# Optimization experiments

Measured on AMD Instinct MI355X. Metric: run time of the kernel, lower is better.

The kernel has to match this reference:

```python
import jax, jax.numpy as jnp
import numpy as np

D_MODEL = 768
N_HEADS = 12
D_K = D_MODEL // N_HEADS
B, S = 2, 2048
EPS = 1e-5  # torch LayerNorm default


def setup_inputs() -> dict:
    key = jax.random.key(0)
    ks = jax.random.split(key, 12)
    sc = 1.0 / np.sqrt(D_MODEL)
    inp = {
        "q": jax.random.normal(ks[0], (B, S, D_MODEL), jnp.float32),
        "k": jax.random.normal(ks[1], (B, S, D_MODEL), jnp.float32),
        "v": jax.random.normal(ks[2], (B, S, D_MODEL), jnp.float32),
        # causal mask: 1 = keep, 0 = masked
        "mask": jnp.tril(jnp.ones((S, S), jnp.int32))[None, None, :, :],
        "Wq": jax.random.normal(ks[3], (D_MODEL, D_MODEL), jnp.float32) * sc,
        "bq": jnp.zeros((D_MODEL,), jnp.float32),
        "Wk": jax.random.normal(ks[4], (D_MODEL, D_MODEL), jnp.float32) * sc,
        "bk": jnp.zeros((D_MODEL,), jnp.float32),
        "Wv": jax.random.normal(ks[5], (D_MODEL, D_MODEL), jnp.float32) * sc,
        "bv": jnp.zeros((D_MODEL,), jnp.float32),
        "Wo": jax.random.normal(ks[6], (D_MODEL, D_MODEL), jnp.float32) * sc,
        "bo": jnp.zeros((D_MODEL,), jnp.float32),
        "gamma": jnp.ones((D_MODEL,), jnp.float32),
        "beta": jnp.zeros((D_MODEL,), jnp.float32),
    }
    return inp


def _layernorm(x, gamma, beta):
    mu = jnp.mean(x, axis=-1, keepdims=True)
    var = jnp.mean(jnp.square(x - mu), axis=-1, keepdims=True)
    return (x - mu) * jax.lax.rsqrt(var + EPS) * gamma + beta


def reference(q, k, v, mask, Wq, bq, Wk, bk, Wv, bv, Wo, bo, gamma, beta):
    residual = q
    # projections + split heads: [B,S,D] -> [B,H,S,Dk]
    def split_heads(x):
        return x.reshape(B, S, N_HEADS, D_K).transpose(0, 2, 1, 3)
    Q = split_heads(q @ Wq.T + bq)
    K = split_heads(k @ Wk.T + bk)
    V = split_heads(v @ Wv.T + bv)
    scores = jnp.einsum("bhqd,bhkd->bhqk", Q, K) / jnp.sqrt(jnp.float32(D_K))
    scores = jnp.where(mask == 0, -jnp.inf, scores)
    attn = jax.nn.softmax(scores, axis=-1)
    # dropout is identity in eval mode
    out = jnp.einsum("bhqk,bhkd->bhqd", attn, V)
    out = out.transpose(0, 2, 1, 3).reshape(B, S, D_MODEL)
    out = out @ Wo.T + bo
    out = _layernorm(residual + out, gamma, beta)
    return (out, attn)
```

## Files before the change

### kernel.cpp

```cpp
#include <hip/hip_runtime.h>
#include <math.h>

typedef __attribute__((ext_vector_type(8))) short bf8_t;
typedef __attribute__((ext_vector_type(4))) float f4_t;

#define MFMA(a,b,c) __builtin_amdgcn_mfma_f32_16x16x32_bf16(a,b,c,0,0,0)

static constexpr int S_ = 2048;
static constexpr size_t QKV_ELEMS = 3145728;
static constexpr size_t W_ELEMS   = 589824;
static constexpr size_t OUT0_ELEMS = 3145728;

__device__ __forceinline__ unsigned short f2bf(float f) {
    union { float f; unsigned u; } v; v.f = f;
    unsigned u = v.u;
    u += 0x7fffu + ((u >> 16) & 1u);
    return (unsigned short)(u >> 16);
}

struct CvtP { const float* s[7]; unsigned short* d[7]; int n[7]; };

__global__ __launch_bounds__(256)
void cvt_all(CvtP p)
{
    const int z = blockIdx.z;
    const int i = (blockIdx.x * 256 + threadIdx.x) * 8;
    if (i >= p.n[z]) return;
    const float* s = p.s[z] + i;
    float4 a = *(const float4*)s, b = *(const float4*)(s + 4);
    uint4 u;
    u.x = (unsigned)f2bf(a.x) | ((unsigned)f2bf(a.y) << 16);
    u.y = (unsigned)f2bf(a.z) | ((unsigned)f2bf(a.w) << 16);
    u.z = (unsigned)f2bf(b.x) | ((unsigned)f2bf(b.y) << 16);
    u.w = (unsigned)f2bf(b.z) | ((unsigned)f2bf(b.w) << 16);
    *(uint4*)(p.d[z] + i) = u;
}

struct GemmP {
    const short* A[3]; const short* W[3]; const float* bias[3];
    void* C[3]; float scale[3]; int mode[3];
};

__global__ __launch_bounds__(256)
void gemm_bf16(GemmP p)
{
    const int z = blockIdx.z;
    const short* __restrict__ A = p.A[z];
    const short* __restrict__ W = p.W[z];
    const float* __restrict__ bias = p.bias[z];
    const float scale = p.scale[z];
    const int mode = p.mode[z];

    __shared__ short As[128 * 40];
    __shared__ short Bs[128 * 40];

    const int t = threadIdx.x;
    const int m0 = blockIdx.y * 128, n0 = blockIdx.x * 128;
    const int w = t >> 6, lane = t & 63, li = lane & 15, qd = lane >> 4;
    const int wm = (w & 1) * 64, wn = (w >> 1) * 64;

    f4_t acc[4][4];
    #pragma unroll
    for (int i = 0; i < 4; ++i)
        #pragma unroll
        for (int j = 0; j < 4; ++j)
            #pragma unroll
            for (int r = 0; r < 4; ++r) acc[i][j][r] = 0.f;

    for (int k0 = 0; k0 < 768; k0 += 32) {
        #pragma unroll
        for (int e = 0; e < 2; ++e) {
            int v = t + e * 256;
            int r = v >> 2, c = (v & 3) * 8;
            *(float4*)&As[r * 40 + c] = *(const float4*)&A[(size_t)(m0 + r) * 768 + k0 + c];
            *(float4*)&Bs[r * 40 + c] = *(const float4*)&W[(size_t)(n0 + r) * 768 + k0 + c];
        }
        __syncthreads();
        bf8_t af[4], bf[4];
        #pragma unroll
        for (int i = 0; i < 4; ++i) af[i] = *(const bf8_t*)&As[(wm + i * 16 + li) * 40 + qd * 8];
        #pragma unroll
        for (int j = 0; j < 4; ++j) bf[j] = *(const bf8_t*)&Bs[(wn + j * 16 + li) * 40 + qd * 8];
        #pragma unroll
        for (int i = 0; i < 4; ++i)
            #pragma unroll
            for (int j = 0; j < 4; ++j)
                acc[i][j] = MFMA(af[i], bf[j], acc[i][j]);
        __syncthreads();
    }

    #pragma unroll
    for (int i = 0; i < 4; ++i) {
        const int row = m0 + wm + i * 16 + qd * 4;
        #pragma unroll
        for (int j = 0; j < 4; ++j) {
            const int col = n0 + wn + j * 16 + li;
            const float bv = bias[col];
            float vals[4];
            #pragma unroll
            for (int r = 0; r < 4; ++r) vals[r] = (acc[i][j][r] + bv) * scale;
            if (mode == 0) {
                #pragma unroll
                for (int r = 0; r < 4; ++r) {
                    const int rr = row + r;
                    int bh = (rr >> 11) * 12 + (col >> 6);
                    ((unsigned short*)p.C[z])[((size_t)bh * 2048 + (rr & 2047)) * 64 + (col & 63)] = f2bf(vals[r]);
                }
            } else if (mode == 1) {
                int bh = (row >> 11) * 12 + (col >> 6);
                ushort4 u;
                u.x = f2bf(vals[0]); u.y = f2bf(vals[1]);
                u.z = f2bf(vals[2]); u.w = f2bf(vals[3]);
                *(ushort4*)&((unsigned short*)p.C[z])[(size_t)(bh * 64 + (col & 63)) * 2048 + (row & 2047)] = u;
            } else {
                #pragma unroll
                for (int r = 0; r < 4; ++r)
                    ((float*)p.C[z])[(size_t)(row + r) * 768 + col] = vals[r];
            }
        }
    }
}

__global__ __launch_bounds__(256)
void attn_fused(const short* __restrict__ Qb, const short* __restrict__ Kb,
                const short* __restrict__ Vt, float* __restrict__ attn,
                unsigned short* __restrict__ AO)
{
    const int qt = 31 - blockIdx.x;
    const int bh = blockIdx.y;
    const int t = threadIdx.x;
    const int ws = t >> 6;
    const int lane = t & 63;
    const int li = lane & 15, qd = lane >> 4;

    __shared__ short Ks[2][4096];
    __shared__ short Vs[2][4096];
    __shared__ short Ps[4][1024];

    const int q0 = qt * 64 + ws * 16;
    const short* Qp = Qb + ((size_t)bh * 2048 + q0 + li) * 64;
    const bf8_t qf0 = *(const bf8_t*)&Qp[qd * 8];
    const bf8_t qf1 = *(const bf8_t*)&Qp[32 + qd * 8];

    const short* Kbh = Kb + (size_t)bh * 2048 * 64;
    const short* Vbh = Vt + (size_t)bh * 64 * 2048;
    float* attnp = attn + (size_t)bh * 2048 * 2048;
    short* Psw = Ps[ws];

    const int r0 = t >> 3, c0 = t & 7;
    const int csw = ((c0 ^ (r0 & 7)) << 3);
    const int lsw = li & 7;

    const float NEG = -1e30f;
    float m_[4] = {NEG, NEG, NEG, NEG}, l_[4] = {0.f, 0.f, 0.f, 0.f};

    {
        float4 ka = *(const float4*)&Kbh[(size_t)r0 * 64 + (c0 << 3)];
        float4 kb_ = *(const float4*)&Kbh[(size_t)(r0 + 32) * 64 + (c0 << 3)];
        *(float4*)&Ks[0][r0 * 64 + csw] = ka;
        *(float4*)&Ks[0][(r0 + 32) * 64 + csw] = kb_;
        int cur = 0;
        for (int kt = 0; kt <= qt; ++kt) {
            float4 na, nb;
            if (kt < qt) {
                na = *(const float4*)&Kbh[(size_t)((kt + 1) * 64 + r0) * 64 + (c0 << 3)];
                nb = *(const float4*)&Kbh[(size_t)((kt + 1) * 64 + r0 + 32) * 64 + (c0 << 3)];
            }
            __syncthreads();
            const short* Kc = Ks[cur];
            bf8_t kf0[4], kf1[4];
            #pragma unroll
            for (int sub = 0; sub < 4; ++sub) {
                const int kr = sub * 16 + li;
                kf0[sub] = *(const bf8_t*)&Kc[kr * 64 + ((qd ^ lsw) << 3)];
                kf1[sub] = *(const bf8_t*)&Kc[kr * 64 + (((4 + qd) ^ lsw) << 3)];
            }
            f4_t c[4];
            #pragma unroll
            for (int sub = 0; sub < 4; ++sub) {
                f4_t z; z[0] = z[1] = z[2] = z[3] = 0.f;
                z = MFMA(qf0, kf0[sub], z);
                z = MFMA(qf1, kf1[sub], z);
                c[sub] = z;
            }
            if (kt == qt) {
                #pragma unroll
                for (int sub = 0; sub < 4; ++sub)
                    #pragma unroll
                    for (int r = 0; r < 4; ++r)
                        if (sub * 16 + li > ws * 16 + qd * 4 + r) c[sub][r] = NEG;
            }
            #pragma unroll
            for (int r = 0; r < 4; ++r) {
                float tm = fmaxf(fmaxf(c[0][r], c[1][r]), fmaxf(c[2][r], c[3][r]));
                float nm = fmaxf(m_[r], tm);
                float s = __expf(c[0][r] - nm) + __expf(c[1][r] - nm)
                        + __expf(c[2][r] - nm) + __expf(c[3][r] - nm);
                l_[r] = l_[r] * __expf(m_[r] - nm) + s;
                m_[r] = nm;
            }
            if (kt < qt) {
                *(float4*)&Ks[cur ^ 1][r0 * 64 + csw] = na;
                *(float4*)&Ks[cur ^ 1][(r0 + 32) * 64 + csw] = nb;
                cur ^= 1;
            }
        }
    }

    float invl[4];
    #pragma unroll
    for (int r = 0; r < 4; ++r) {
        float mg = m_[r];
        mg = fmaxf(mg, __shfl_xor(mg, 1, 64));
        mg = fmaxf(mg, __shfl_xor(mg, 2, 64));
        mg = fmaxf(mg, __shfl_xor(mg, 4, 64));
        mg = fmaxf(mg, __shfl_xor(mg, 8, 64));
        float lg = l_[r] * __expf(m_[r] - mg);
        lg += __shfl_xor(lg, 1, 64);
        lg += __shfl_xor(lg, 2, 64);
        lg += __shfl_xor(lg, 4, 64);
        lg += __shfl_xor(lg, 8, 64);
        m_[r] = mg;
        invl[r] = 1.f / lg;
    }

    f4_t o[4];
    #pragma unroll
    for (int d = 0; d < 4; ++d)
        #pragma unroll
        for (int r = 0; r < 4; ++r) o[d][r] = 0.f;

    {
        float4 ka = *(const float4*)&Kbh[(size_t)r0 * 64 + (c0 << 3)];
        float4 kb_ = *(const float4*)&Kbh[(size_t)(r0 + 32) * 64 + (c0 << 3)];
        float4 va = *(const float4*)&Vbh[(size_t)r0 * 2048 + (c0 << 3)];
        float4 vc_ = *(const float4*)&Vbh[(size_t)(r0 + 32) * 2048 + (c0 << 3)];
        __syncthreads();
        *(float4*)&Ks[0][r0 * 64 + csw] = ka;
        *(float4*)&Ks[0][(r0 + 32) * 64 + csw] = kb_;
        *(float4*)&Vs[0][r0 * 64 + csw] = va;
        *(float4*)&Vs[0][(r0 + 32) * 64 + csw] = vc_;
        int cur = 0;
        for (int kt = 0; kt <= qt; ++kt) {
            float4 nka, nkb, nva, nvb;
            if (kt < qt) {
                nka = *(const float4*)&Kbh[(size_t)((kt + 1) * 64 + r0) * 64 + (c0 << 3)];
                nkb = *(const float4*)&Kbh[(size_t)((kt + 1) * 64 + r0 + 32) * 64 + (c0 << 3)];
                nva = *(const float4*)&Vbh[(size_t)r0 * 2048 + (kt + 1) * 64 + (c0 << 3)];
                nvb = *(const float4*)&Vbh[(size_t)(r0 + 32) * 2048 + (kt + 1) * 64 + (c0 << 3)];
            }
            __syncthreads();
            const short* Kc = Ks[cur];
            const short* Vc = Vs[cur];
            bf8_t kf0[4], kf1[4];
            #pragma unroll
            for (int sub = 0; sub < 4; ++sub) {
                const int kr = sub * 16 + li;
                kf0[sub] = *(const bf8_t*)&Kc[kr * 64 + ((qd ^ lsw) << 3)];
                kf1[sub] = *(const bf8_t*)&Kc[kr * 64 + (((4 + qd) ^ lsw) << 3)];
            }
            f4_t c[4];
            #pragma unroll
            for (int sub = 0; sub < 4; ++sub) {
                f4_t z; z[0] = z[1] = z[2] = z[3] = 0.f;
                z = MFMA(qf0, kf0[sub], z);
                z = MFMA(qf1, kf1[sub], z);
                c[sub] = z;
            }
            if (kt == qt) {
                #pragma unroll
                for (int sub = 0; sub < 4; ++sub)
                    #pragma unroll
                    for (int r = 0; r < 4; ++r)
                        if (sub * 16 + li > ws * 16 + qd * 4 + r) c[sub][r] = NEG;
            }
            #pragma unroll
            for (int sub = 0; sub < 4; ++sub)
                #pragma unroll
                for (int r = 0; r < 4; ++r) {
                    const float pe = __expf(c[sub][r] - m_[r]) * invl[r];
                    attnp[(size_t)(q0 + qd * 4 + r) * 2048 + kt * 64 + sub * 16 + li] = pe;
                    const int prow = qd * 4 + r;
                    const int pcol = sub * 16 + li;
                    Psw[prow * 64 + (((pcol >> 3) ^ (prow & 7)) << 3) + (pcol & 7)] = (short)f2bf(pe);
                }
            #pragma unroll
            for (int h = 0; h < 2; ++h) {
                bf8_t pa = *(const bf8_t*)&Psw[li * 64 + (((h * 4 + qd) ^ lsw) << 3)];
                #pragma unroll
                for (int d = 0; d < 4; ++d) {
                    bf8_t vf = *(const bf8_t*)&Vc[(d * 16 + li) * 64 + (((h * 4 + qd) ^ lsw) << 3)];
                    o[d] = MFMA(pa, vf, o[d]);
                }
            }
            if (kt < qt) {
                *(float4*)&Ks[cur ^ 1][r0 * 64 + csw] = nka;
                *(float4*)&Ks[cur ^ 1][(r0 + 32) * 64 + csw] = nkb;
                *(float4*)&Vs[cur ^ 1][r0 * 64 + csw] = nva;
                *(float4*)&Vs[cur ^ 1][(r0 + 32) * 64 + csw] = nvb;
                cur ^= 1;
            }
        }
    }

    const int w4 = (31 - qt) * 16;
    const float4 z4 = make_float4(0.f, 0.f, 0.f, 0.f);
    for (int r = 0; r < 16; ++r) {
        float* rp = &attnp[(size_t)(q0 + r) * 2048 + (qt + 1) * 64];
        for (int cc = lane; cc < w4; cc += 64)
            *(float4*)&rp[cc * 4] = z4;
    }

    const int b = bh / 12, h_ = bh % 12;
    #pragma unroll
    for (int d = 0; d < 4; ++d)
        #pragma unroll
        for (int r = 0; r < 4; ++r)
            AO[(size_t)(b * 2048 + q0 + qd * 4 + r) * 768 + h_ * 64 + d * 16 + li] = f2bf(o[d][r]);
}

__global__ __launch_bounds__(256)
void ln_kernel(const float* __restrict__ resid, const float* __restrict__ proj,
               const float* __restrict__ gamma, const float* __restrict__ beta,
               float* __restrict__ out)
{
    __shared__ float red[4];
    const int row = blockIdx.x, t = threadIdx.x;
    const size_t base = (size_t)row * 768;
    float x[3];
    float s = 0.f;
    #pragma unroll
    for (int e = 0; e < 3; ++e) {
        int j = t + e * 256;
        x[e] = resid[base + j] + proj[base + j];
        s += x[e];
    }
    #pragma unroll
    for (int off = 1; off < 64; off <<= 1) s += __shfl_xor(s, off, 64);
    if ((t & 63) == 0) red[t >> 6] = s;
    __syncthreads();
    s = red[0] + red[1] + red[2] + red[3];
    const float mu = s * (1.f / 768.f);
    float vs = 0.f;
    #pragma unroll
    for (int e = 0; e < 3; ++e) { float d = x[e] - mu; vs += d * d; }
    __syncthreads();
    #pragma unroll
    for (int off = 1; off < 64; off <<= 1) vs += __shfl_xor(vs, off, 64);
    if ((t & 63) == 0) red[t >> 6] = vs;
    __syncthreads();
    vs = red[0] + red[1] + red[2] + red[3];
    const float inv = rsqrtf(vs * (1.f / 768.f) + 1e-5f);
    #pragma unroll
    for (int e = 0; e < 3; ++e) {
        int j = t + e * 256;
        out[base + j] = (x[e] - mu) * inv * gamma[j] + beta[j];
    }
}

extern "C" void kernel_launch(void* const* d_in, const int* in_sizes, int n_in,
                              void* d_out, int out_size, void* d_ws, size_t ws_size,
                              hipStream_t stream)
{
    const float* q     = (const float*)d_in[0];
    const float* k     = (const float*)d_in[1];
    const float* v     = (const float*)d_in[2];
    const float* Wq    = (const float*)d_in[4];
    const float* bq    = (const float*)d_in[5];
    const float* Wk    = (const float*)d_in[6];
    const float* bk    = (const float*)d_in[7];
    const float* Wv    = (const float*)d_in[8];
    const float* bv    = (const float*)d_in[9];
    const float* Wo    = (const float*)d_in[10];
    const float* bo    = (const float*)d_in[11];
    const float* gamma = (const float*)d_in[12];
    const float* beta  = (const float*)d_in[13];

    float* out  = (float*)d_out;
    float* attn = out + OUT0_ELEMS;

    short* qc  = (short*)d_ws;
    short* kc  = qc + QKV_ELEMS;
    short* vc  = kc + QKV_ELEMS;
    short* wqc = vc + QKV_ELEMS;
    short* wkc = wqc + W_ELEMS;
    short* wvc = wkc + W_ELEMS;
    short* woc = wvc + W_ELEMS;
    short* Qb  = woc + W_ELEMS;
    short* Kb  = Qb + QKV_ELEMS;
    short* Vt  = Kb + QKV_ELEMS;
    short* AO  = Vt + QKV_ELEMS;
    float* P   = (float*)(AO + QKV_ELEMS);

    CvtP cp;
    cp.s[0] = q;  cp.d[0] = (unsigned short*)qc;  cp.n[0] = (int)QKV_ELEMS;
    cp.s[1] = k;  cp.d[1] = (unsigned short*)kc;  cp.n[1] = (int)QKV_ELEMS;
    cp.s[2] = v;  cp.d[2] = (unsigned short*)vc;  cp.n[2] = (int)QKV_ELEMS;
    cp.s[3] = Wq; cp.d[3] = (unsigned short*)wqc; cp.n[3] = (int)W_ELEMS;
    cp.s[4] = Wk; cp.d[4] = (unsigned short*)wkc; cp.n[4] = (int)W_ELEMS;
    cp.s[5] = Wv; cp.d[5] = (unsigned short*)wvc; cp.n[5] = (int)W_ELEMS;
    cp.s[6] = Wo; cp.d[6] = (unsigned short*)woc; cp.n[6] = (int)W_ELEMS;
    cvt_all<<<dim3(1536, 1, 7), 256, 0, stream>>>(cp);

    GemmP gp;
    gp.A[0] = qc; gp.W[0] = wqc; gp.bias[0] = bq; gp.C[0] = Qb; gp.scale[0] = 0.125f; gp.mode[0] = 0;
    gp.A[1] = kc; gp.W[1] = wkc; gp.bias[1] = bk; gp.C[1] = Kb; gp.scale[1] = 1.f;    gp.mode[1] = 0;
    gp.A[2] = vc; gp.W[2] = wvc; gp.bias[2] = bv; gp.C[2] = Vt; gp.scale[2] = 1.f;    gp.mode[2] = 1;
    gemm_bf16<<<dim3(6, 32, 3), 256, 0, stream>>>(gp);

    attn_fused<<<dim3(32, 24), 256, 0, stream>>>(Qb, Kb, Vt, attn, (unsigned short*)AO);

    GemmP gp2;
    gp2.A[0] = AO; gp2.W[0] = woc; gp2.bias[0] = bo; gp2.C[0] = P; gp2.scale[0] = 1.f; gp2.mode[0] = 2;
    gp2.A[1] = gp2.A[2] = AO; gp2.W[1] = gp2.W[2] = woc; gp2.bias[1] = gp2.bias[2] = bo;
    gp2.C[1] = gp2.C[2] = P; gp2.scale[1] = gp2.scale[2] = 1.f; gp2.mode[1] = gp2.mode[2] = 2;
    gemm_bf16<<<dim3(6, 32, 1), 256, 0, stream>>>(gp2);

    ln_kernel<<<dim3(4096), 256, 0, stream>>>(q, P, gamma, beta, out);
}
```

Before: 595.5 us.

## Make attention persistent with atomic work queue and use direct-to-LDS GEMM loads

The attention kernel becomes persistent: 640 blocks pull (query-tile, batch-head) work items from a global atomic counter, heaviest causal tiles first. This is meant to improve load balance across the triangular workload and cut tail effects; `cvt_all` resets the counter. MFMA sections also get raised wave priority via `s_setprio`. The projection GEMM now loads tiles straight into LDS with `global_load_lds` and drops the row padding, which saves register staging but may add LDS bank conflicts on fragment reads.

```diff
diff --git a/kernel.cpp b/kernel.cpp
--- a/kernel.cpp
+++ b/kernel.cpp
@@ -18,12 +18,19 @@
     return (unsigned short)(u >> 16);
 }
 
-struct CvtP { const float* s[7]; unsigned short* d[7]; int n[7]; };
+__device__ __forceinline__ void gload_lds16(const short* g, short* l) {
+    __builtin_amdgcn_global_load_lds((const __attribute__((address_space(1))) void*)g,
+                                     (__attribute__((address_space(3))) void*)l,
+                                     16, 0, 0);
+}
+
+struct CvtP { const float* s[7]; unsigned short* d[7]; int n[7]; int* ctr; };
 
 __global__ __launch_bounds__(256)
 void cvt_all(CvtP p)
 {
     const int z = blockIdx.z;
+    if (z == 0 && blockIdx.x == 0 && threadIdx.x == 0) *p.ctr = 0;
     const int i = (blockIdx.x * 256 + threadIdx.x) * 8;
     if (i >= p.n[z]) return;
     const float* s = p.s[z] + i;
@@ -51,8 +58,8 @@
     const float scale = p.scale[z];
     const int mode = p.mode[z];
 
-    __shared__ short As[128 * 40];
-    __shared__ short Bs[128 * 40];
+    __shared__ short As[128 * 32];
+    __shared__ short Bs[128 * 32];
 
     const int t = threadIdx.x;
     const int m0 = blockIdx.y * 128, n0 = blockIdx.x * 128;
@@ -70,17 +77,17 @@
     for (int k0 = 0; k0 < 768; k0 += 32) {
         #pragma unroll
         for (int e = 0; e < 2; ++e) {
-            int v = t + e * 256;
-            int r = v >> 2, c = (v & 3) * 8;
-            *(float4*)&As[r * 40 + c] = *(const float4*)&A[(size_t)(m0 + r) * 768 + k0 + c];
-            *(float4*)&Bs[r * 40 + c] = *(const float4*)&W[(size_t)(n0 + r) * 768 + k0 + c];
+            const int ch = t + e * 256;
+            const int r = ch >> 2, c = (ch & 3) << 3;
+            gload_lds16(&A[(size_t)(m0 + r) * 768 + k0 + c], &As[ch << 3]);
+            gload_lds16(&W[(size_t)(n0 + r) * 768 + k0 + c], &Bs[ch << 3]);
         }
         __syncthreads();
         bf8_t af[4], bf[4];
         #pragma unroll
-        for (int i = 0; i < 4; ++i) af[i] = *(const bf8_t*)&As[(wm + i * 16 + li) * 40 + qd * 8];
-        #pragma unroll
-        for (int j = 0; j < 4; ++j) bf[j] = *(const bf8_t*)&Bs[(wn + j * 16 + li) * 40 + qd * 8];
+        for (int i = 0; i < 4; ++i) af[i] = *(const bf8_t*)&As[(wm + i * 16 + li) * 32 + qd * 8];
+        #pragma unroll
+        for (int j = 0; j < 4; ++j) bf[j] = *(const bf8_t*)&Bs[(wn + j * 16 + li) * 32 + qd * 8];
         #pragma unroll
         for (int i = 0; i < 4; ++i)
             #pragma unroll
@@ -124,199 +131,212 @@
 __global__ __launch_bounds__(256)
 void attn_fused(const short* __restrict__ Qb, const short* __restrict__ Kb,
                 const short* __restrict__ Vt, float* __restrict__ attn,
-                unsigned short* __restrict__ AO)
+                unsigned short* __restrict__ AO, int* __restrict__ ctr)
 {
-    const int qt = 31 - blockIdx.x;
-    const int bh = blockIdx.y;
+    __shared__ short Ks[2][4096];
+    __shared__ short Vs[2][4096];
+    __shared__ short Ps[4][1024];
+    __shared__ int sh_j;
+
     const int t = threadIdx.x;
     const int ws = t >> 6;
     const int lane = t & 63;
     const int li = lane & 15, qd = lane >> 4;
-
-    __shared__ short Ks[2][4096];
-    __shared__ short Vs[2][4096];
-    __shared__ short Ps[4][1024];
-
-    const int q0 = qt * 64 + ws * 16;
-    const short* Qp = Qb + ((size_t)bh * 2048 + q0 + li) * 64;
-    const bf8_t qf0 = *(const bf8_t*)&Qp[qd * 8];
-    const bf8_t qf1 = *(const bf8_t*)&Qp[32 + qd * 8];
-
-    const short* Kbh = Kb + (size_t)bh * 2048 * 64;
-    const short* Vbh = Vt + (size_t)bh * 64 * 2048;
-    float* attnp = attn + (size_t)bh * 2048 * 2048;
-    short* Psw = Ps[ws];
-
     const int r0 = t >> 3, c0 = t & 7;
     const int csw = ((c0 ^ (r0 & 7)) << 3);
     const int lsw = li & 7;
-
     const float NEG = -1e30f;
-    float m_[4] = {NEG, NEG, NEG, NEG}, l_[4] = {0.f, 0.f, 0.f, 0.f};
-
-    {
-        float4 ka = *(const float4*)&Kbh[(size_t)r0 * 64 + (c0 << 3)];
-        float4 kb_ = *(const float4*)&Kbh[(size_t)(r0 + 32) * 64 + (c0 << 3)];
-        *(float4*)&Ks[0][r0 * 64 + csw] = ka;
-        *(float4*)&Ks[0][(r0 + 32) * 64 + csw] = kb_;
-        int cur = 0;
-        for (int kt = 0; kt <= qt; ++kt) {
-            float4 na, nb;
-            if (kt < qt) {
-                na = *(const float4*)&Kbh[(size_t)((kt + 1) * 64 + r0) * 64 + (c0 << 3)];
-                nb = *(const float4*)&Kbh[(size_t)((kt + 1) * 64 + r0 + 32) * 64 + (c0 << 3)];
+
+    for (;;) {
+        if (t == 0) sh_j = atomicAdd(ctr, 1);
+        __syncthreads();
+        const int j = sh_j;
+        if (j >= 768) return;
+        const int qt = 31 - (j / 24);
+        const int bh = j % 24;
+
+        const int q0 = qt * 64 + ws * 16;
+        const short* Qp = Qb + ((size_t)bh * 2048 + q0 + li) * 64;
+        const bf8_t qf0 = *(const bf8_t*)&Qp[qd * 8];
+        const bf8_t qf1 = *(const bf8_t*)&Qp[32 + qd * 8];
+
+        const short* Kbh = Kb + (size_t)bh * 2048 * 64;
+        const short* Vbh = Vt + (size_t)bh * 64 * 2048;
+        float* attnp = attn + (size_t)bh * 2048 * 2048;
+        short* Psw = Ps[ws];
+
+        float m_[4] = {NEG, NEG, NEG, NEG}, l_[4] = {0.f, 0.f, 0.f, 0.f};
+
+        {
+            float4 ka = *(const float4*)&Kbh[(size_t)r0 * 64 + (c0 << 3)];
+            float4 kb_ = *(const float4*)&Kbh[(size_t)(r0 + 32) * 64 + (c0 << 3)];
+            *(float4*)&Ks[0][r0 * 64 + csw] = ka;
+            *(float4*)&Ks[0][(r0 + 32) * 64 + csw] = kb_;
+            int cur = 0;
+            for (int kt = 0; kt <= qt; ++kt) {
+                float4 na, nb;
+                if (kt < qt) {
+                    na = *(const float4*)&Kbh[(size_t)((kt + 1) * 64 + r0) * 64 + (c0 << 3)];
+                    nb = *(const float4*)&Kbh[(size_t)((kt + 1) * 64 + r0 + 32) * 64 + (c0 << 3)];
+                }
+                __syncthreads();
+                const short* Kc = Ks[cur];
+                bf8_t kf0[4], kf1[4];
+                #pragma unroll
+                for (int sub = 0; sub < 4; ++sub) {
+                    const int kr = sub * 16 + li;
+                    kf0[sub] = *(const bf8_t*)&Kc[kr * 64 + ((qd ^ lsw) << 3)];
+                    kf1[sub] = *(const bf8_t*)&Kc[kr * 64 + (((4 + qd) ^ lsw) << 3)];
+                }
+                f4_t c[4];
+                __builtin_amdgcn_s_setprio(1);
+                #pragma unroll
+                for (int sub = 0; sub < 4; ++sub) {
+                    f4_t z; z[0] = z[1] = z[2] = z[3] = 0.f;
+                    z = MFMA(qf0, kf0[sub], z);
+                    z = MFMA(qf1, kf1[sub], z);
+                    c[sub] = z;
+                }
+                __builtin_amdgcn_s_setprio(0);
+                if (kt == qt) {
+                    #pragma unroll
+                    for (int sub = 0; sub < 4; ++sub)
+                        #pragma unroll
+                        for (int r = 0; r < 4; ++r)
+                            if (sub * 16 + li > ws * 16 + qd * 4 + r) c[sub][r] = NEG;
+                }
+                #pragma unroll
+                for (int r = 0; r < 4; ++r) {
+                    float tm = fmaxf(fmaxf(c[0][r], c[1][r]), fmaxf(c[2][r], c[3][r]));
+                    float nm = fmaxf(m_[r], tm);
+                    float s = __expf(c[0][r] - nm) + __expf(c[1][r] - nm)
+                            + __expf(c[2][r] - nm) + __expf(c[3][r] - nm);
+                    l_[r] = l_[r] * __expf(m_[r] - nm) + s;
+                    m_[r] = nm;
+                }
+                if (kt < qt) {
+                    *(float4*)&Ks[cur ^ 1][r0 * 64 + csw] = na;
+                    *(float4*)&Ks[cur ^ 1][(r0 + 32) * 64 + csw] = nb;
+                    cur ^= 1;
+                }
             }
+        }
+
+        float invl[4];
+        #pragma unroll
+        for (int r = 0; r < 4; ++r) {
+            float mg = m_[r];
+            mg = fmaxf(mg, __shfl_xor(mg, 1, 64));
+            mg = fmaxf(mg, __shfl_xor(mg, 2, 64));
+            mg = fmaxf(mg, __shfl_xor(mg, 4, 64));
+            mg = fmaxf(mg, __shfl_xor(mg, 8, 64));
+            float lg = l_[r] * __expf(m_[r] - mg);
+            lg += __shfl_xor(lg, 1, 64);
+            lg += __shfl_xor(lg, 2, 64);
+            lg += __shfl_xor(lg, 4, 64);
+            lg += __shfl_xor(lg, 8, 64);
+            m_[r] = mg;
+            invl[r] = 1.f / lg;
+        }
+
+        f4_t o[4];
+        #pragma unroll
+        for (int d = 0; d < 4; ++d)
+            #pragma unroll
+            for (int r = 0; r < 4; ++r) o[d][r] = 0.f;
+
+        {
+            float4 ka = *(const float4*)&Kbh[(size_t)r0 * 64 + (c0 << 3)];
+            float4 kb_ = *(const float4*)&Kbh[(size_t)(r0 + 32) * 64 + (c0 << 3)];
+            float4 va = *(const float4*)&Vbh[(size_t)r0 * 2048 + (c0 << 3)];
+            float4 vc_ = *(const float4*)&Vbh[(size_t)(r0 + 32) * 2048 + (c0 << 3)];
             __syncthreads();
-            const short* Kc = Ks[cur];
-            bf8_t kf0[4], kf1[4];
-            #pragma unroll
-            for (int sub = 0; sub < 4; ++sub) {
-                const int kr = sub * 16 + li;
-                kf0[sub] = *(const bf8_t*)&Kc[kr * 64 + ((qd ^ lsw) << 3)];
-                kf1[sub] = *(const bf8_t*)&Kc[kr * 64 + (((4 + qd) ^ lsw) << 3)];
-            }
-            f4_t c[4];
-            #pragma unroll
-            for (int sub = 0; sub < 4; ++sub) {
-                f4_t z; z[0] = z[1] = z[2] = z[3] = 0.f;
-                z = MFMA(qf0, kf0[sub], z);
-                z = MFMA(qf1, kf1[sub], z);
-                c[sub] = z;
-            }
-            if (kt == qt) {
+            *(float4*)&Ks[0][r0 * 64 + csw] = ka;
+            *(float4*)&Ks[0][(r0 + 32) * 64 + csw] = kb_;
+            *(float4*)&Vs[0][r0 * 64 + csw] = va;
+            *(float4*)&Vs[0][(r0 + 32) * 64 + csw] = vc_;
+            int cur = 0;
+            for (int kt = 0; kt <= qt; ++kt) {
+                float4 nka, nkb, nva, nvb;
+                if (kt < qt) {
+                    nka = *(const float4*)&Kbh[(size_t)((kt + 1) * 64 + r0) * 64 + (c0 << 3)];
+                    nkb = *(const float4*)&Kbh[(size_t)((kt + 1) * 64 + r0 + 32) * 64 + (c0 << 3)];
+                    nva = *(const float4*)&Vbh[(size_t)r0 * 2048 + (kt + 1) * 64 + (c0 << 3)];
+                    nvb = *(const float4*)&Vbh[(size_t)(r0 + 32) * 2048 + (kt + 1) * 64 + (c0 << 3)];
+                }
+                __syncthreads();
+                const short* Kc = Ks[cur];
+                const short* Vc = Vs[cur];
+                bf8_t kf0[4], kf1[4];
+                #pragma unroll
+                for (int sub = 0; sub < 4; ++sub) {
+                    const int kr = sub * 16 + li;
+                    kf0[sub] = *(const bf8_t*)&Kc[kr * 64 + ((qd ^ lsw) << 3)];
+                    kf1[sub] = *(const bf8_t*)&Kc[kr * 64 + (((4 + qd) ^ lsw) << 3)];
+                }
+                f4_t c[4];
+                __builtin_amdgcn_s_setprio(1);
+                #pragma unroll
+                for (int sub = 0; sub < 4; ++sub) {
+                    f4_t z; z[0] = z[1] = z[2] = z[3] = 0.f;
+                    z = MFMA(qf0, kf0[sub], z);
+                    z = MFMA(qf1, kf1[sub], z);
+                    c[sub] = z;
+                }
+                __builtin_amdgcn_s_setprio(0);
+                if (kt == qt) {
+                    #pragma unroll
+                    for (int sub = 0; sub < 4; ++sub)
+                        #pragma unroll
+                        for (int r = 0; r < 4; ++r)
+                            if (sub * 16 + li > ws * 16 + qd * 4 + r) c[sub][r] = NEG;
+                }
                 #pragma unroll
                 for (int sub = 0; sub < 4; ++sub)
                     #pragma unroll
-                    for (int r = 0; r < 4; ++r)
-                        if (sub * 16 + li > ws * 16 + qd * 4 + r) c[sub][r] = NEG;
+                    for (int r = 0; r < 4; ++r) {
+                        const float pe = __expf(c[sub][r] - m_[r]) * invl[r];
+                        attnp[(size_t)(q0 + qd * 4 + r) * 2048 + kt * 64 + sub * 16 + li] = pe;
+                        const int prow = qd * 4 + r;
+                        const int pcol = sub * 16 + li;
+                        Psw[prow * 64 + (((pcol >> 3) ^ (prow & 7)) << 3) + (pcol & 7)] = (short)f2bf(pe);
+                    }
+                __builtin_amdgcn_s_setprio(1);
+                #pragma unroll
+                for (int h = 0; h < 2; ++h) {
+                    bf8_t pa = *(const bf8_t*)&Psw[li * 64 + (((h * 4 + qd) ^ lsw) << 3)];
+                    #pragma unroll
+                    for (int d = 0; d < 4; ++d) {
+                        bf8_t vf = *(const bf8_t*)&Vc[(d * 16 + li) * 64 + (((h * 4 + qd) ^ lsw) << 3)];
+                        o[d] = MFMA(pa, vf, o[d]);
+                    }
+                }
+                __builtin_amdgcn_s_setprio(0);
+                if (kt < qt) {
+                    *(float4*)&Ks[cur ^ 1][r0 * 64 + csw] = nka;
+                    *(float4*)&Ks[cur ^ 1][(r0 + 32) * 64 + csw] = nkb;
+                    *(float4*)&Vs[cur ^ 1][r0 * 64 + csw] = nva;
+                    *(float4*)&Vs[cur ^ 1][(r0 + 32) * 64 + csw] = nvb;
+                    cur ^= 1;
+                }
             }
+        }
+
+        const int w4 = (31 - qt) * 16;
+        const float4 z4 = make_float4(0.f, 0.f, 0.f, 0.f);
+        for (int r = 0; r < 16; ++r) {
+            float* rp = &attnp[(size_t)(q0 + r) * 2048 + (qt + 1) * 64];
+            for (int cc = lane; cc < w4; cc += 64)
+                *(float4*)&rp[cc * 4] = z4;
+        }
+
+        const int b = bh / 12, h_ = bh % 12;
+        #pragma unroll
+        for (int d = 0; d < 4; ++d)
             #pragma unroll
-            for (int r = 0; r < 4; ++r) {
-                float tm = fmaxf(fmaxf(c[0][r], c[1][r]), fmaxf(c[2][r], c[3][r]));
-                float nm = fmaxf(m_[r], tm);
-                float s = __expf(c[0][r] - nm) + __expf(c[1][r] - nm)
-                        + __expf(c[2][r] - nm) + __expf(c[3][r] - nm);
-                l_[r] = l_[r] * __expf(m_[r] - nm) + s;
-                m_[r] = nm;
-            }
-            if (kt < qt) {
-                *(float4*)&Ks[cur ^ 1][r0 * 64 + csw] = na;
-                *(float4*)&Ks[cur ^ 1][(r0 + 32) * 64 + csw] = nb;
-                cur ^= 1;
-            }
-        }
+            for (int r = 0; r < 4; ++r)
+                AO[(size_t)(b * 2048 + q0 + qd * 4 + r) * 768 + h_ * 64 + d * 16 + li] = f2bf(o[d][r]);
     }
-
-    float invl[4];
-    #pragma unroll
-    for (int r = 0; r < 4; ++r) {
-        float mg = m_[r];
-        mg = fmaxf(mg, __shfl_xor(mg, 1, 64));
-        mg = fmaxf(mg, __shfl_xor(mg, 2, 64));
-        mg = fmaxf(mg, __shfl_xor(mg, 4, 64));
-        mg = fmaxf(mg, __shfl_xor(mg, 8, 64));
-        float lg = l_[r] * __expf(m_[r] - mg);
-        lg += __shfl_xor(lg, 1, 64);
-        lg += __shfl_xor(lg, 2, 64);
-        lg += __shfl_xor(lg, 4, 64);
-        lg += __shfl_xor(lg, 8, 64);
-        m_[r] = mg;
-        invl[r] = 1.f / lg;
-    }
-
-    f4_t o[4];
-    #pragma unroll
-    for (int d = 0; d < 4; ++d)
-        #pragma unroll
-        for (int r = 0; r < 4; ++r) o[d][r] = 0.f;
-
-    {
-        float4 ka = *(const float4*)&Kbh[(size_t)r0 * 64 + (c0 << 3)];
-        float4 kb_ = *(const float4*)&Kbh[(size_t)(r0 + 32) * 64 + (c0 << 3)];
-        float4 va = *(const float4*)&Vbh[(size_t)r0 * 2048 + (c0 << 3)];
-        float4 vc_ = *(const float4*)&Vbh[(size_t)(r0 + 32) * 2048 + (c0 << 3)];
-        __syncthreads();
-        *(float4*)&Ks[0][r0 * 64 + csw] = ka;
-        *(float4*)&Ks[0][(r0 + 32) * 64 + csw] = kb_;
-        *(float4*)&Vs[0][r0 * 64 + csw] = va;
-        *(float4*)&Vs[0][(r0 + 32) * 64 + csw] = vc_;
-        int cur = 0;
-        for (int kt = 0; kt <= qt; ++kt) {
-            float4 nka, nkb, nva, nvb;
-            if (kt < qt) {
-                nka = *(const float4*)&Kbh[(size_t)((kt + 1) * 64 + r0) * 64 + (c0 << 3)];
-                nkb = *(const float4*)&Kbh[(size_t)((kt + 1) * 64 + r0 + 32) * 64 + (c0 << 3)];
-                nva = *(const float4*)&Vbh[(size_t)r0 * 2048 + (kt + 1) * 64 + (c0 << 3)];
-                nvb = *(const float4*)&Vbh[(size_t)(r0 + 32) * 2048 + (kt + 1) * 64 + (c0 << 3)];
-            }
-            __syncthreads();
-            const short* Kc = Ks[cur];
-            const short* Vc = Vs[cur];
-            bf8_t kf0[4], kf1[4];
-            #pragma unroll
-            for (int sub = 0; sub < 4; ++sub) {
-                const int kr = sub * 16 + li;
-                kf0[sub] = *(const bf8_t*)&Kc[kr * 64 + ((qd ^ lsw) << 3)];
-                kf1[sub] = *(const bf8_t*)&Kc[kr * 64 + (((4 + qd) ^ lsw) << 3)];
-            }
-            f4_t c[4];
-            #pragma unroll
-            for (int sub = 0; sub < 4; ++sub) {
-                f4_t z; z[0] = z[1] = z[2] = z[3] = 0.f;
-                z = MFMA(qf0, kf0[sub], z);
-                z = MFMA(qf1, kf1[sub], z);
-                c[sub] = z;
-            }
-            if (kt == qt) {
-                #pragma unroll
-                for (int sub = 0; sub < 4; ++sub)
-                    #pragma unroll
-                    for (int r = 0; r < 4; ++r)
-                        if (sub * 16 + li > ws * 16 + qd * 4 + r) c[sub][r] = NEG;
-            }
-            #pragma unroll
-            for (int sub = 0; sub < 4; ++sub)
-                #pragma unroll
-                for (int r = 0; r < 4; ++r) {
-                    const float pe = __expf(c[sub][r] - m_[r]) * invl[r];
-                    attnp[(size_t)(q0 + qd * 4 + r) * 2048 + kt * 64 + sub * 16 + li] = pe;
-                    const int prow = qd * 4 + r;
-                    const int pcol = sub * 16 + li;
-                    Psw[prow * 64 + (((pcol >> 3) ^ (prow & 7)) << 3) + (pcol & 7)] = (short)f2bf(pe);
-                }
-            #pragma unroll
-            for (int h = 0; h < 2; ++h) {
-                bf8_t pa = *(const bf8_t*)&Psw[li * 64 + (((h * 4 + qd) ^ lsw) << 3)];
-                #pragma unroll
-                for (int d = 0; d < 4; ++d) {
-                    bf8_t vf = *(const bf8_t*)&Vc[(d * 16 + li) * 64 + (((h * 4 + qd) ^ lsw) << 3)];
-                    o[d] = MFMA(pa, vf, o[d]);
-                }
-            }
-            if (kt < qt) {
-                *(float4*)&Ks[cur ^ 1][r0 * 64 + csw] = nka;
-                *(float4*)&Ks[cur ^ 1][(r0 + 32) * 64 + csw] = nkb;
-                *(float4*)&Vs[cur ^ 1][r0 * 64 + csw] = nva;
-                *(float4*)&Vs[cur ^ 1][(r0 + 32) * 64 + csw] = nvb;
-                cur ^= 1;
-            }
-        }
-    }
-
-    const int w4 = (31 - qt) * 16;
-    const float4 z4 = make_float4(0.f, 0.f, 0.f, 0.f);
-    for (int r = 0; r < 16; ++r) {
-        float* rp = &attnp[(size_t)(q0 + r) * 2048 + (qt + 1) * 64];
-        for (int cc = lane; cc < w4; cc += 64)
-            *(float4*)&rp[cc * 4] = z4;
-    }
-
-    const int b = bh / 12, h_ = bh % 12;
-    #pragma unroll
-    for (int d = 0; d < 4; ++d)
-        #pragma unroll
-        for (int r = 0; r < 4; ++r)
-            AO[(size_t)(b * 2048 + q0 + qd * 4 + r) * 768 + h_ * 64 + d * 16 + li] = f2bf(o[d][r]);
 }
 
 __global__ __launch_bounds__(256)
@@ -391,6 +411,7 @@
     short* Vt  = Kb + QKV_ELEMS;
     short* AO  = Vt + QKV_ELEMS;
     float* P   = (float*)(AO + QKV_ELEMS);
+    int*   ctr = (int*)(P + OUT0_ELEMS);
 
     CvtP cp;
     cp.s[0] = q;  cp.d[0] = (unsigned short*)qc;  cp.n[0] = (int)QKV_ELEMS;
@@ -400,6 +421,7 @@
     cp.s[4] = Wk; cp.d[4] = (unsigned short*)wkc; cp.n[4] = (int)W_ELEMS;
     cp.s[5] = Wv; cp.d[5] = (unsigned short*)wvc; cp.n[5] = (int)W_ELEMS;
     cp.s[6] = Wo; cp.d[6] = (unsigned short*)woc; cp.n[6] = (int)W_ELEMS;
+    cp.ctr = ctr;
     cvt_all<<<dim3(1536, 1, 7), 256, 0, stream>>>(cp);
 
     GemmP gp;
@@ -408,7 +430,7 @@
     gp.A[2] = vc; gp.W[2] = wvc; gp.bias[2] = bv; gp.C[2] = Vt; gp.scale[2] = 1.f;    gp.mode[2] = 1;
     gemm_bf16<<<dim3(6, 32, 3), 256, 0, stream>>>(gp);
 
-    attn_fused<<<dim3(32, 24), 256, 0, stream>>>(Qb, Kb, Vt, attn, (unsigned short*)AO);
+    attn_fused<<<dim3(640), 256, 0, stream>>>(Qb, Kb, Vt, attn, (unsigned short*)AO, ctr);
 
     GemmP gp2;
     gp2.A[0] = AO; gp2.W[0] = woc; gp2.bias[0] = bo; gp2.C[0] = P; gp2.scale[0] = 1.f; gp2.mode[0] = 2;
```

After: 610.2 us. 2.5% more time.
